# Performance work log

Hardware: AMD Instinct MI355X
Metric: run time of the kernel (lower is better)

Reference implementation:

```python
import jax, jax.numpy as jnp
import numpy as np

KERNEL_SIZE = 9  # spatial kernel extent used only for output cropping


def setup_inputs() -> dict:
    key = jax.random.key(0)
    k1, k2, k3, k4 = jax.random.split(key, 4)
    B, Cin, Cout, H, W = 32, 64, 128, 128, 128
    Wf = W // 2 + 1  # rfft bins on last dim (W even, no pad branch)
    return {
        "signal": jax.random.normal(k1, (B, Cin, H, W), dtype=jnp.float32),
        "weight_real": jax.random.normal(k2, (Cout, Cin, H, Wf), dtype=jnp.float32),
        "weight_imag": jax.random.normal(k3, (Cout, Cin, H, Wf), dtype=jnp.float32),
        "bias": jax.random.normal(k4, (Cout,), dtype=jnp.float32),
    }


def reference(signal, weight_real, weight_imag, bias):
    # FFT conv with a frequency-domain complex kernel (groups=1, padding=0,
    # stride=1). Matches torch fft_conv: rfftn -> complex matmul over channels
    # per frequency bin -> irfftn -> crop -> bias add.
    B, Cin, H, W = signal.shape
    sig_fr = jnp.fft.rfftn(signal, axes=(2, 3))            # [B, Cin, H, W//2+1] c64
    kernel = (weight_real + 1j * weight_imag).astype(jnp.complex64)
    # complex_matmul with groups=1: contract Cin per (h,w) frequency bin
    out_fr = jnp.einsum('bihw,oihw->bohw', sig_fr, kernel)  # [B, Cout, H, W//2+1]
    out = jnp.fft.irfftn(out_fr, axes=(2, 3))               # [B, Cout, H, W] real
    Ho = H - KERNEL_SIZE + 1
    Wo = W - KERNEL_SIZE + 1
    out = out[:, :, :Ho, :Wo]
    out = out + bias[None, :, None, None]
    return out
```

## Files before the change

kernel.cpp:

```cpp
#include <hip/hip_runtime.h>
#include <math.h>

#define DI __device__ __forceinline__

constexpr int Hh   = 128;
constexpr int Ww   = 128;
constexpr int WF   = 65;
constexpr int NBIN = Hh * WF;
constexpr int NB   = 32;
constexpr int CIN  = 64;
constexpr int COUT = 128;
constexpr int HO   = 120;
constexpr int WO   = 120;

typedef __bf16 bf16x8 __attribute__((ext_vector_type(8)));
typedef float  f32x16 __attribute__((ext_vector_type(16)));

DI unsigned int bfbits(float x) {
  unsigned int u = __float_as_uint(x);
  return (u + 0x7FFFu + ((u >> 16) & 1u)) >> 16;
}
DI unsigned int packbf(float re, float im) { return bfbits(re) | (bfbits(im) << 16); }
DI float2 unpackbf(unsigned int v) {
  return make_float2(__uint_as_float(v << 16), __uint_as_float(v & 0xFFFF0000u));
}

DI f32x16 MFMA32(uint4 a, uint4 b, f32x16 c) {
  return __builtin_amdgcn_mfma_f32_32x32x16_bf16(
      __builtin_bit_cast(bf16x8, a), __builtin_bit_cast(bf16x8, b), c, 0, 0, 0);
}
DI unsigned int rotneg(unsigned int x) { return ((x << 16) | (x >> 16)) ^ 0x80000000u; }
DI uint4 derive(uint4 s) {
  uint4 r; r.x = rotneg(s.x); r.y = rotneg(s.y); r.z = rotneg(s.z); r.w = rotneg(s.w);
  return r;
}

DI void wsync() {
  asm volatile("s_waitcnt lgkmcnt(0)" ::: "memory");
  __builtin_amdgcn_sched_barrier(0);
}

DI int bitrev6(int l) {
  return ((l & 1) << 5) | ((l & 2) << 3) | ((l & 4) << 1) |
         ((l & 8) >> 1) | ((l & 16) >> 3) | ((l & 32) >> 5);
}
DI float2 cmul(float2 a, float2 b) {
  return make_float2(a.x * b.x - a.y * b.y, a.x * b.y + a.y * b.x);
}
DI float2 sxor(float2 v, int m) {
  return make_float2(__shfl_xor(v.x, m), __shfl_xor(v.y, m));
}
DI void stg(float2& v, int h, float2 tw, int l) {
  float2 p = sxor(v, h);
  float2 s = make_float2(v.x + p.x, v.y + p.y);
  float2 d = make_float2(p.x - v.x, p.y - v.y);
  float2 m = cmul(d, tw);
  v = (l & h) ? m : s;
}
DI void stg1(float2& v, int l) {
  float2 p = sxor(v, 1);
  v = (l & 1) ? make_float2(p.x - v.x, p.y - v.y)
              : make_float2(v.x + p.x, v.y + p.y);
}
DI void twinit(float2* tw, int l) {
  float s_, c_;
  sincosf(-(float)M_PI * (float)l / 64.f, &s_, &c_);
  tw[0] = make_float2(c_, s_);
#pragma unroll
  for (int i = 0; i < 5; ++i) {
    const int h = 32 >> i;
    sincosf(-(float)M_PI * (float)(l & (h - 1)) / (float)h, &s_, &c_);
    tw[1 + i] = make_float2(c_, s_);
  }
}
DI void sfft128x2(float2& a0, float2& b0, float2& a1, float2& b1,
                  const float2* tw, int l) {
  {
    float2 s = make_float2(a0.x + b0.x, a0.y + b0.y);
    float2 d = make_float2(a0.x - b0.x, a0.y - b0.y);
    a0 = s; b0 = cmul(d, tw[0]);
  }
  {
    float2 s = make_float2(a1.x + b1.x, a1.y + b1.y);
    float2 d = make_float2(a1.x - b1.x, a1.y - b1.y);
    a1 = s; b1 = cmul(d, tw[0]);
  }
#pragma unroll
  for (int i = 0; i < 5; ++i) {
    const int h = 32 >> i;
    stg(a0, h, tw[1 + i], l); stg(a1, h, tw[1 + i], l);
    stg(b0, h, tw[1 + i], l); stg(b1, h, tw[1 + i], l);
  }
  stg1(a0, l); stg1(a1, l); stg1(b0, l); stg1(b1, l);
}

__global__ __launch_bounds__(256) void fwd_fft(const float* __restrict__ sig,
                                               unsigned int* __restrict__ sf) {
  __shared__ unsigned int sImg[NBIN];
  __shared__ __align__(16) float2 rowbuf[4][2][128];

  const int t = threadIdx.x, grp = t >> 6, l = t & 63;
  const size_t img = blockIdx.x;
  const float* src = sig + img * (size_t)(Hh * Ww);
  unsigned int* dst = sf + img * (size_t)NBIN;

  float2 tw[6]; twinit(tw, l);
  const int br = bitrev6(l);

  for (int batch = 0; batch < 8; ++batch) {
    float2 a[2], b[2];
#pragma unroll
    for (int f = 0; f < 2; ++f) {
      const int jp = batch * 8 + grp * 2 + f;
      const float* r0 = src + (size_t)(2 * jp) * Ww;
      a[f] = make_float2(r0[l],      r0[Ww + l]);
      b[f] = make_float2(r0[64 + l], r0[Ww + 64 + l]);
    }
    sfft128x2(a[0], b[0], a[1], b[1], tw, l);
#pragma unroll
    for (int f = 0; f < 2; ++f) {
      *(float4*)&rowbuf[grp][f][2 * br] =
          make_float4(a[f].x, a[f].y, b[f].x, b[f].y);
    }
    wsync();
#pragma unroll
    for (int f = 0; f < 2; ++f) {
      const int jp = batch * 8 + grp * 2 + f;
      float2 Zk = rowbuf[grp][f][l];
      float2 Zm = rowbuf[grp][f][(128 - l) & 127];
      sImg[(2 * jp) * WF + l]     = packbf(0.5f * (Zk.x + Zm.x), 0.5f * (Zk.y - Zm.y));
      sImg[(2 * jp + 1) * WF + l] = packbf(0.5f * (Zk.y + Zm.y), 0.5f * (Zm.x - Zk.x));
      if (l == 0) {
        float2 Z64 = rowbuf[grp][f][64];
        sImg[(2 * jp) * WF + 64]     = packbf(Z64.x, 0.f);
        sImg[(2 * jp + 1) * WF + 64] = packbf(Z64.y, 0.f);
      }
    }
    wsync();
  }
  __syncthreads();

  for (int batch = 0; batch < 9; ++batch) {
    float2 a[2], b[2]; int wcol[2];
#pragma unroll
    for (int f = 0; f < 2; ++f) {
      const int w = batch * 8 + grp * 2 + f; wcol[f] = w;
      const int wc = (w < WF) ? w : (WF - 1);
      a[f] = unpackbf(sImg[l * WF + wc]);
      b[f] = unpackbf(sImg[(l + 64) * WF + wc]);
    }
    sfft128x2(a[0], b[0], a[1], b[1], tw, l);
#pragma unroll
    for (int f = 0; f < 2; ++f) {
      if (wcol[f] < WF) {
        sImg[(2 * br) * WF + wcol[f]]     = packbf(a[f].x, a[f].y);
        sImg[(2 * br + 1) * WF + wcol[f]] = packbf(b[f].x, b[f].y);
      }
    }
  }
  __syncthreads();

  const uint4* s4 = (const uint4*)sImg;
  uint4* d4 = (uint4*)dst;
  for (int idx = t; idx < NBIN / 4; idx += 256) d4[idx] = s4[idx];
}

constexpr int PT    = 16;
constexpr int PLANE = 260;

__global__ __launch_bounds__(512, 3) void spec_mm(const unsigned int* __restrict__ sf,
                                                  const float* __restrict__ wr,
                                                  const float* __restrict__ wi,
                                                  unsigned int* __restrict__ of) {
  __shared__ unsigned int wbuf[PT * PLANE];
  __shared__ unsigned int sbuf[PT * PLANE];

  const int t = threadIdx.x;
  const int bid = blockIdx.x;
  const int swz = (bid & 7) * 260 + (bid >> 3);
  const int o0 = (swz & 3) * 32;
  const int p0 = (swz >> 2) * PT;

  const int po = t & 3;
  const int ii = (t >> 2) & 7;
  const int rl = (t >> 5) & 15;

  const float* wrp0 = wr + ((size_t)(o0 + rl) * CIN + ii) * NBIN + p0 + po * 4;
  const float* wip0 = wi + ((size_t)(o0 + rl) * CIN + ii) * NBIN + p0 + po * 4;
  const unsigned int* sfp0 = sf + ((size_t)rl * CIN + ii) * NBIN + p0 + po * 4;
  const size_t rowAdv = (size_t)16 * CIN * NBIN;

  auto slotOf = [](int row, int i) {
    return ((((row * 2) + (i >> 2)) ^ ((row >> 2) & 7)) << 2) + (i & 3);
  };
  const int slotLo = slotOf(rl, ii);
  const int slotHi = slotOf(rl + 16, ii);

  const int l = t & 63, wv = t >> 6;
  const int lr = l & 31, lq = l >> 5;
  const int moff = ((((lr * 2) + lq) ^ ((lr >> 2) & 7)) << 2);
  const int pA = 2 * wv, pB = 2 * wv + 1;

  f32x16 aR0 = {}, aI0 = {}, aR1 = {}, aI1 = {};

  float4 w0r[2], w1r[2], w0i[2], w1i[2]; uint4 s0v[2], s1v[2];

#pragma unroll
  for (int s = 0; s < 2; ++s) {
    const size_t adv = (size_t)s * 8 * NBIN;
    w0r[s] = *(const float4*)(wrp0 + adv);  w1r[s] = *(const float4*)(wrp0 + adv + rowAdv);
    w0i[s] = *(const float4*)(wip0 + adv);  w1i[s] = *(const float4*)(wip0 + adv + rowAdv);
    s0v[s] = *(const uint4*)(sfp0 + adv);   s1v[s] = *(const uint4*)(sfp0 + adv + rowAdv);
  }

#pragma unroll
  for (int kq = 0; kq < 8; ++kq) {
    const int cs = kq & 1;
    {
      const float* a0 = (const float*)&w0r[cs]; const float* a1 = (const float*)&w1r[cs];
      const float* b0 = (const float*)&w0i[cs]; const float* b1 = (const float*)&w1i[cs];
      const unsigned int* u0 = (const unsigned int*)&s0v[cs];
      const unsigned int* u1 = (const unsigned int*)&s1v[cs];
#pragma unroll
      for (int j = 0; j < 4; ++j) {
        const int pp = (po * 4 + j) * PLANE;
        wbuf[pp + slotLo] = packbf(a0[j], -b0[j]);
        wbuf[pp + slotHi] = packbf(a1[j], -b1[j]);
        sbuf[pp + slotLo] = u0[j];
        sbuf[pp + slotHi] = u1[j];
      }
    }
    if (kq < 6) {
      const size_t adv = (size_t)(kq + 2) * 8 * NBIN;
      w0r[cs] = *(const float4*)(wrp0 + adv);  w1r[cs] = *(const float4*)(wrp0 + adv + rowAdv);
      w0i[cs] = *(const float4*)(wip0 + adv);  w1i[cs] = *(const float4*)(wip0 + adv + rowAdv);
      s0v[cs] = *(const uint4*)(sfp0 + adv);   s1v[cs] = *(const uint4*)(sfp0 + adv + rowAdv);
    }
    __syncthreads();

    {
      const uint4 a = *(const uint4*)&wbuf[pA * PLANE + moff];
      const uint4 s = *(const uint4*)&sbuf[pA * PLANE + moff];
      aR0 = MFMA32(a, s, aR0);
      aI0 = MFMA32(a, derive(s), aI0);
    }
    {
      const uint4 a = *(const uint4*)&wbuf[pB * PLANE + moff];
      const uint4 s = *(const uint4*)&sbuf[pB * PLANE + moff];
      aR1 = MFMA32(a, s, aR1);
      aI1 = MFMA32(a, derive(s), aI1);
    }
    __syncthreads();
  }

  const int b = lr;
#pragma unroll
  for (int r = 0; r < 16; ++r) {
    const int o = o0 + (r & 3) + 8 * (r >> 2) + 4 * lq;
    uint2 v;
    v.x = packbf(aR0[r], aI0[r]);
    v.y = packbf(aR1[r], aI1[r]);
    *(uint2*)(of + ((size_t)b * COUT + o) * NBIN + p0 + 2 * wv) = v;
  }
}

__global__ __launch_bounds__(256) void inv_fft(const unsigned int* __restrict__ of,
                                               const float* __restrict__ bias,
                                               float* __restrict__ out) {
  __shared__ unsigned int sImg[NBIN];

  const int t = threadIdx.x, grp = t >> 6, l = t & 63;
  const size_t img = blockIdx.x;
  const unsigned int* src = of + img * (size_t)NBIN;
  float* dst = out + img * (size_t)(HO * WO);
  const float bo = bias[img & (COUT - 1)];

  float2 tw[6]; twinit(tw, l);
  const int br = bitrev6(l);

  const uint4* s4 = (const uint4*)src;
  uint4* d4 = (uint4*)sImg;
  for (int idx = t; idx < NBIN / 4; idx += 256) d4[idx] = s4[idx];
  __syncthreads();

  for (int batch = 0; batch < 9; ++batch) {
    float2 a[2], b[2]; int wcol[2];
#pragma unroll
    for (int f = 0; f < 2; ++f) {
      const int w = batch * 8 + grp * 2 + f; wcol[f] = w;
      const int wc = (w < WF) ? w : (WF - 1);
      float2 za = unpackbf(sImg[l * WF + wc]);
      float2 zb = unpackbf(sImg[(l + 64) * WF + wc]);
      a[f] = make_float2(za.x, -za.y);
      b[f] = make_float2(zb.x, -zb.y);
    }
    sfft128x2(a[0], b[0], a[1], b[1], tw, l);
#pragma unroll
    for (int f = 0; f < 2; ++f) {
      if (wcol[f] < WF) {
        sImg[(2 * br) * WF + wcol[f]]     = packbf(a[f].x, -a[f].y);
        sImg[(2 * br + 1) * WF + wcol[f]] = packbf(b[f].x, -b[f].y);
      }
    }
  }
  __syncthreads();

  const float sc = 1.f / 16384.f;
  for (int batch = 0; batch < 8; ++batch) {
    float2 a[2], b[2]; int jpv[2];
#pragma unroll
    for (int f = 0; f < 2; ++f) {
      const int jp = batch * 8 + grp * 2 + f; jpv[f] = jp;
      const int jc = (jp < 60) ? jp : 59;
      const unsigned int* X0p = &sImg[(size_t)(2 * jc) * WF];
      const unsigned int* X1p = X0p + WF;
      float2 za, zb;
      if (l == 0) {
        za = make_float2(unpackbf(X0p[0]).x,  unpackbf(X1p[0]).x);
        zb = make_float2(unpackbf(X0p[64]).x, unpackbf(X1p[64]).x);
      } else {
        float2 x0 = unpackbf(X0p[l]), x1 = unpackbf(X1p[l]);
        za = make_float2(x0.x - x1.y, x0.y + x1.x);
        const int mI = 64 - l;
        float2 y0 = unpackbf(X0p[mI]), y1 = unpackbf(X1p[mI]);
        zb = make_float2(y0.x + y1.y, y1.x - y0.y);
      }
      a[f] = make_float2(za.x, -za.y);
      b[f] = make_float2(zb.x, -zb.y);
    }
    sfft128x2(a[0], b[0], a[1], b[1], tw, l);
    const int n0 = 2 * br;
#pragma unroll
    for (int f = 0; f < 2; ++f) {
      const int jp = jpv[f];
      if (jp < 60 && n0 < WO) {
        float2 r0 = make_float2(a[f].x * sc + bo,  b[f].x * sc + bo);
        float2 r1 = make_float2(-a[f].y * sc + bo, -b[f].y * sc + bo);
        *(float2*)(dst + (size_t)(2 * jp) * WO + n0)     = r0;
        *(float2*)(dst + (size_t)(2 * jp + 1) * WO + n0) = r1;
      }
    }
  }
}

extern "C" void kernel_launch(void* const* d_in, const int* in_sizes, int n_in,
                              void* d_out, int out_size, void* d_ws, size_t ws_size,
                              hipStream_t stream) {
  const float* signal = (const float*)d_in[0];
  const float* wr     = (const float*)d_in[1];
  const float* wi     = (const float*)d_in[2];
  const float* bias   = (const float*)d_in[3];
  float* out = (float*)d_out;

  unsigned int* sig_fr = (unsigned int*)d_out;
  unsigned int* out_fr = (unsigned int*)d_ws;
  (void)in_sizes; (void)n_in; (void)out_size; (void)ws_size;

  fwd_fft<<<NB * CIN, 256, 0, stream>>>(signal, sig_fr);
  spec_mm<<<2080, 512, 0, stream>>>(sig_fr, wr, wi, out_fr);
  inv_fft<<<NB * COUT, 256, 0, stream>>>(out_fr, bias, out);
}
```

Before: 517.0 us.

## Use bpermute for FFT unscramble, fast sincos, and single-buffer spec_mm prefetch

The forward FFT no longer routes the bit-reversed row spectrum through a shared-memory row buffer with explicit waits. Lanes fetch their k and 128-k partners directly with ds_bpermute, and twiddle setup uses the fast __sincosf intrinsic. In spec_mm the two-deep register prefetch becomes a single-deep one, and the launch bound asks for 4 blocks per CU instead of 3, trading prefetch depth for occupancy. Fast sincos slightly lowers twiddle accuracy, and the shallower prefetch may expose more global-load latency.

```diff
diff --git a/kernel.cpp b/kernel.cpp
--- a/kernel.cpp
+++ b/kernel.cpp
@@ -35,11 +35,6 @@
   return r;
 }
 
-DI void wsync() {
-  asm volatile("s_waitcnt lgkmcnt(0)" ::: "memory");
-  __builtin_amdgcn_sched_barrier(0);
-}
-
 DI int bitrev6(int l) {
   return ((l & 1) << 5) | ((l & 2) << 3) | ((l & 4) << 1) |
          ((l & 8) >> 1) | ((l & 16) >> 3) | ((l & 32) >> 5);
@@ -49,6 +44,9 @@
 }
 DI float2 sxor(float2 v, int m) {
   return make_float2(__shfl_xor(v.x, m), __shfl_xor(v.y, m));
+}
+DI float bpermf(int addr, float v) {
+  return __int_as_float(__builtin_amdgcn_ds_bpermute(addr, __float_as_int(v)));
 }
 DI void stg(float2& v, int h, float2 tw, int l) {
   float2 p = sxor(v, h);
@@ -64,12 +62,12 @@
 }
 DI void twinit(float2* tw, int l) {
   float s_, c_;
-  sincosf(-(float)M_PI * (float)l / 64.f, &s_, &c_);
+  __sincosf(-(float)M_PI * (float)l / 64.f, &s_, &c_);
   tw[0] = make_float2(c_, s_);
 #pragma unroll
   for (int i = 0; i < 5; ++i) {
     const int h = 32 >> i;
-    sincosf(-(float)M_PI * (float)(l & (h - 1)) / (float)h, &s_, &c_);
+    __sincosf(-(float)M_PI * (float)(l & (h - 1)) / (float)h, &s_, &c_);
     tw[1 + i] = make_float2(c_, s_);
   }
 }
@@ -97,7 +95,6 @@
 __global__ __launch_bounds__(256) void fwd_fft(const float* __restrict__ sig,
                                                unsigned int* __restrict__ sf) {
   __shared__ unsigned int sImg[NBIN];
-  __shared__ __align__(16) float2 rowbuf[4][2][128];
 
   const int t = threadIdx.x, grp = t >> 6, l = t & 63;
   const size_t img = blockIdx.x;
@@ -106,6 +103,10 @@
 
   float2 tw[6]; twinit(tw, l);
   const int br = bitrev6(l);
+  const int sk4 = bitrev6(l >> 1) * 4;
+  const int im  = (128 - l) & 127;
+  const int sm4 = bitrev6(im >> 1) * 4;
+  const bool podd = (l & 1) != 0;
 
   for (int batch = 0; batch < 8; ++batch) {
     float2 a[2], b[2];
@@ -119,24 +120,21 @@
     sfft128x2(a[0], b[0], a[1], b[1], tw, l);
 #pragma unroll
     for (int f = 0; f < 2; ++f) {
-      *(float4*)&rowbuf[grp][f][2 * br] =
-          make_float4(a[f].x, a[f].y, b[f].x, b[f].y);
-    }
-    wsync();
-#pragma unroll
-    for (int f = 0; f < 2; ++f) {
       const int jp = batch * 8 + grp * 2 + f;
-      float2 Zk = rowbuf[grp][f][l];
-      float2 Zm = rowbuf[grp][f][(128 - l) & 127];
+      float axk = bpermf(sk4, a[f].x), ayk = bpermf(sk4, a[f].y);
+      float bxk = bpermf(sk4, b[f].x), byk = bpermf(sk4, b[f].y);
+      float axm = bpermf(sm4, a[f].x), aym = bpermf(sm4, a[f].y);
+      float bxm = bpermf(sm4, b[f].x), bym = bpermf(sm4, b[f].y);
+      float z64x = bpermf(4, a[f].x),  z64y = bpermf(4, a[f].y);
+      float2 Zk = podd ? make_float2(bxk, byk) : make_float2(axk, ayk);
+      float2 Zm = podd ? make_float2(bxm, bym) : make_float2(axm, aym);
       sImg[(2 * jp) * WF + l]     = packbf(0.5f * (Zk.x + Zm.x), 0.5f * (Zk.y - Zm.y));
       sImg[(2 * jp + 1) * WF + l] = packbf(0.5f * (Zk.y + Zm.y), 0.5f * (Zm.x - Zk.x));
       if (l == 0) {
-        float2 Z64 = rowbuf[grp][f][64];
-        sImg[(2 * jp) * WF + 64]     = packbf(Z64.x, 0.f);
-        sImg[(2 * jp + 1) * WF + 64] = packbf(Z64.y, 0.f);
-      }
-    }
-    wsync();
+        sImg[(2 * jp) * WF + 64]     = packbf(z64x, 0.f);
+        sImg[(2 * jp + 1) * WF + 64] = packbf(z64y, 0.f);
+      }
+    }
   }
   __syncthreads();
 
@@ -168,7 +166,7 @@
 constexpr int PT    = 16;
 constexpr int PLANE = 260;
 
-__global__ __launch_bounds__(512, 3) void spec_mm(const unsigned int* __restrict__ sf,
+__global__ __launch_bounds__(512, 4) void spec_mm(const unsigned int* __restrict__ sf,
                                                   const float* __restrict__ wr,
                                                   const float* __restrict__ wi,
                                                   unsigned int* __restrict__ of) {
@@ -203,38 +201,31 @@
 
   f32x16 aR0 = {}, aI0 = {}, aR1 = {}, aI1 = {};
 
-  float4 w0r[2], w1r[2], w0i[2], w1i[2]; uint4 s0v[2], s1v[2];
-
-#pragma unroll
-  for (int s = 0; s < 2; ++s) {
-    const size_t adv = (size_t)s * 8 * NBIN;
-    w0r[s] = *(const float4*)(wrp0 + adv);  w1r[s] = *(const float4*)(wrp0 + adv + rowAdv);
-    w0i[s] = *(const float4*)(wip0 + adv);  w1i[s] = *(const float4*)(wip0 + adv + rowAdv);
-    s0v[s] = *(const uint4*)(sfp0 + adv);   s1v[s] = *(const uint4*)(sfp0 + adv + rowAdv);
-  }
-
-#pragma unroll
+  float4 w0r, w1r, w0i, w1i; uint4 s0v, s1v;
+  {
+    w0r = *(const float4*)(wrp0);          w1r = *(const float4*)(wrp0 + rowAdv);
+    w0i = *(const float4*)(wip0);          w1i = *(const float4*)(wip0 + rowAdv);
+    s0v = *(const uint4*)(sfp0);           s1v = *(const uint4*)(sfp0 + rowAdv);
+  }
+
   for (int kq = 0; kq < 8; ++kq) {
-    const int cs = kq & 1;
-    {
-      const float* a0 = (const float*)&w0r[cs]; const float* a1 = (const float*)&w1r[cs];
-      const float* b0 = (const float*)&w0i[cs]; const float* b1 = (const float*)&w1i[cs];
-      const unsigned int* u0 = (const unsigned int*)&s0v[cs];
-      const unsigned int* u1 = (const unsigned int*)&s1v[cs];
-#pragma unroll
-      for (int j = 0; j < 4; ++j) {
-        const int pp = (po * 4 + j) * PLANE;
-        wbuf[pp + slotLo] = packbf(a0[j], -b0[j]);
-        wbuf[pp + slotHi] = packbf(a1[j], -b1[j]);
-        sbuf[pp + slotLo] = u0[j];
-        sbuf[pp + slotHi] = u1[j];
-      }
-    }
-    if (kq < 6) {
-      const size_t adv = (size_t)(kq + 2) * 8 * NBIN;
-      w0r[cs] = *(const float4*)(wrp0 + adv);  w1r[cs] = *(const float4*)(wrp0 + adv + rowAdv);
-      w0i[cs] = *(const float4*)(wip0 + adv);  w1i[cs] = *(const float4*)(wip0 + adv + rowAdv);
-      s0v[cs] = *(const uint4*)(sfp0 + adv);   s1v[cs] = *(const uint4*)(sfp0 + adv + rowAdv);
+    const float* a0 = (const float*)&w0r;  const float* a1 = (const float*)&w1r;
+    const float* b0 = (const float*)&w0i;  const float* b1 = (const float*)&w1i;
+    const unsigned int* u0 = (const unsigned int*)&s0v;
+    const unsigned int* u1 = (const unsigned int*)&s1v;
+#pragma unroll
+    for (int j = 0; j < 4; ++j) {
+      const int pp = (po * 4 + j) * PLANE;
+      wbuf[pp + slotLo] = packbf(a0[j], -b0[j]);
+      wbuf[pp + slotHi] = packbf(a1[j], -b1[j]);
+      sbuf[pp + slotLo] = u0[j];
+      sbuf[pp + slotHi] = u1[j];
+    }
+    if (kq < 7) {
+      const size_t adv = (size_t)(kq + 1) * 8 * NBIN;
+      w0r = *(const float4*)(wrp0 + adv);  w1r = *(const float4*)(wrp0 + adv + rowAdv);
+      w0i = *(const float4*)(wip0 + adv);  w1i = *(const float4*)(wip0 + adv + rowAdv);
+      s0v = *(const uint4*)(sfp0 + adv);   s1v = *(const uint4*)(sfp0 + adv + rowAdv);
     }
     __syncthreads();
 
```

Result: faster. 489.8 us (-5.3%).
